# Kernel tuning notes

Measured on AMD Instinct MI355X. Metric: run time of the kernel, lower is better.

## Reference

```python
import jax, jax.numpy as jnp
import numpy as np

B, S, D = 2, 2048, 1024
H, DC = 16, 16          # num_heads, head_coord_dim
CD = 16                 # coord_dim
DH = D // H             # head_dim = 64


def setup_inputs() -> dict:
    key = jax.random.key(0)
    ks = jax.random.split(key, 8)
    s = 0.02
    return {
        "hidden_states": jax.random.normal(ks[0], (B, S, D), jnp.float32),
        "coordinates": jax.random.normal(ks[1], (B, S, CD), jnp.float32),
        "Wv": jax.random.normal(ks[2], (D, D), jnp.float32) * s,
        "bv": jnp.zeros((D,), jnp.float32),
        "Wc": jax.random.normal(ks[3], (H * DC, CD), jnp.float32) * s,
        "bc": jnp.zeros((H * DC,), jnp.float32),
        "Wn": jax.random.normal(ks[4], (CD, D), jnp.float32) * s,
        "bn": jnp.zeros((CD,), jnp.float32),
        "Wo": jax.random.normal(ks[5], (D, D), jnp.float32) * s,
        "bo": jnp.zeros((D,), jnp.float32),
        "gamma": jnp.zeros((1, H, 1, 1), jnp.float32),
    }


def reference(hidden_states, coordinates, Wv, bv, Wc, bc, Wn, bn, Wo, bo, gamma):
    # value: [B,S,D] -> [B,H,S,DH]
    value = (hidden_states @ Wv.T + bv).reshape(B, S, H, DH).transpose(0, 2, 1, 3)
    # coordinate heads: [B,S,CD] -> [B,H,S,DC]
    z = (coordinates @ Wc.T + bc).reshape(B, S, H, DC).transpose(0, 2, 1, 3)
    z_sq = jnp.sum(z * z, axis=-1, keepdims=True)           # [B,H,S,1]
    # pairwise squared distances [B,H,S,S]
    sq_dist = z_sq + jnp.swapaxes(z_sq, -1, -2) - 2.0 * jnp.einsum("bhsc,bhtc->bhst", z, z)
    sq_dist = jnp.maximum(sq_dist, 0.0)
    g = jax.nn.softplus(gamma)                               # [1,H,1,1]
    attn = jax.nn.softmax(-g * sq_dist, axis=-1)             # [B,H,S,S]
    out = jnp.einsum("bhst,bhtd->bhsd", attn, value)         # [B,H,S,DH]
    out = out.transpose(0, 2, 1, 3).reshape(B, S, D)
    updated_hidden = out @ Wo.T + bo
    updated_coords = hidden_states @ Wn.T + bn               # [B,S,CD]
    return updated_hidden, updated_coords
```

## Files before the change

kernel.cpp:

```cpp
#include <hip/hip_runtime.h>
#include <math.h>

typedef short short8 __attribute__((ext_vector_type(8)));
typedef short short4t __attribute__((ext_vector_type(4)));
typedef float f32x4  __attribute__((ext_vector_type(4)));

#define AS1 __attribute__((address_space(1)))
#define AS3 __attribute__((address_space(3)))

__device__ __forceinline__ unsigned cvt_pk_bf16(float lo, float hi) {
    unsigned r;
    asm("v_cvt_pk_bf16_f32 %0, %1, %2" : "=v"(r) : "v"(lo), "v"(hi));
    return r;
}
__device__ __forceinline__ unsigned f2bf_rne(float x) {
    unsigned u = __float_as_uint(x);
    return (u + 0x7fffu + ((u >> 16) & 1u)) >> 16;
}
__device__ __forceinline__ float exp2_fast(float x) {
    float r;
    asm("v_exp_f32 %0, %1" : "=v"(r) : "v"(x));
    return r;
}
__device__ __forceinline__ f32x4 mfma_k16(short4t a, short4t b, f32x4 c) {
#if __has_builtin(__builtin_amdgcn_mfma_f32_16x16x16bf16_1k)
    return __builtin_amdgcn_mfma_f32_16x16x16bf16_1k(a, b, c, 0, 0, 0);
#else
    asm volatile("v_mfma_f32_16x16x16_bf16 %0, %1, %2, %0" : "+v"(c) : "v"(a), "v"(b));
    return c;
#endif
}

__global__ __launch_bounds__(256) void f2bf_kernel(const float* __restrict__ in,
                                                   short* __restrict__ out, int n8) {
    const int i = blockIdx.x * 256 + threadIdx.x;
    if (i >= n8) return;
    const float4 a = ((const float4*)in)[2 * i];
    const float4 b = ((const float4*)in)[2 * i + 1];
    uint4 r;
    r.x = cvt_pk_bf16(a.x, a.y);
    r.y = cvt_pk_bf16(a.z, a.w);
    r.z = cvt_pk_bf16(b.x, b.y);
    r.w = cvt_pk_bf16(b.z, b.w);
    ((uint4*)out)[i] = r;
}

__global__ __launch_bounds__(256) void f2bfW(const float* __restrict__ Wv,
                                             const float* __restrict__ Wo,
                                             const float* __restrict__ Wn,
                                             short* __restrict__ Wvb,
                                             short* __restrict__ Wob,
                                             short* __restrict__ Wnb) {
    const int i = blockIdx.x * 256 + threadIdx.x;
    const float* src;
    short* dst;
    int ii;
    if (i < 131072)      { src = Wv; dst = Wvb; ii = i; }
    else if (i < 262144) { src = Wo; dst = Wob; ii = i - 131072; }
    else                 { src = Wn; dst = Wnb; ii = i - 262144; }
    const float4 a = ((const float4*)src)[2 * ii];
    const float4 b = ((const float4*)src)[2 * ii + 1];
    uint4 r;
    r.x = cvt_pk_bf16(a.x, a.y);
    r.y = cvt_pk_bf16(a.z, a.w);
    r.z = cvt_pk_bf16(b.x, b.y);
    r.w = cvt_pk_bf16(b.z, b.w);
    ((uint4*)dst)[ii] = r;
}

__global__ __launch_bounds__(256) void zker3(const float* __restrict__ coords,
                                             const float* __restrict__ Wc,
                                             const float* __restrict__ bc,
                                             const float* __restrict__ gamma,
                                             short* __restrict__ ZA,
                                             short* __restrict__ ZB) {
    const int bs = blockIdx.x;
    const int b = bs >> 11, s = bs & 2047;
    const int tid = threadIdx.x;
    __shared__ float csh[16];
    if (tid < 16) csh[tid] = coords[(size_t)bs * 16 + tid];
    __syncthreads();
    float z = bc[tid];
#pragma unroll
    for (int k = 0; k < 16; k++) z = fmaf(csh[k], Wc[tid * 16 + k], z);
    const unsigned ub = f2bf_rne(z);
    const float zb = __uint_as_float(ub << 16);
    float sq = zb * zb;
    sq += __shfl_xor(sq, 1, 64);
    sq += __shfl_xor(sq, 2, 64);
    sq += __shfl_xor(sq, 4, 64);
    sq += __shfl_xor(sq, 8, 64);
    const int h = tid >> 4, c = tid & 15;
    const float gm = gamma[h];
    const float sp = fmaxf(gm, 0.f) + log1pf(__expf(-fabsf(gm)));
    const float ch = -sp * 1.4426950408889634f;
    const size_t row = ((size_t)(b * 16 + h) * 2048 + s) * 32;
    ZA[row + c] = (short)ub;
    ZA[row + 16 + c] = (c == 0) ? (short)f2bf_rne(sq)
                                : (c == 1 ? (short)0x3F80 : (short)0);
    ZB[row + c] = (short)f2bf_rne(-2.f * ch * zb);
    ZB[row + 16 + c] = (c == 0) ? (short)f2bf_rne(ch)
                                : (c == 1 ? (short)f2bf_rne(ch * sq) : (short)0);
}

template <int EPI>
__global__ __launch_bounds__(256) void gemm_mfma(const short* __restrict__ A,
                                                 const short* __restrict__ W,
                                                 const float* __restrict__ bias,
                                                 void* __restrict__ Cout) {
    __shared__ short As[2][128][64];
    __shared__ short Bs[2][64][64];
    const int tid = threadIdx.x;
    const int wv = tid >> 6, l = tid & 63, g = l >> 4, qc = l & 15;
    const int wm = wv >> 1, wn = wv & 1;
    const int Mb = blockIdx.y * 128, Nb = blockIdx.x * 64;

    auto stage = [&](int buf, int k0) {
#pragma unroll
        for (int i = 0; i < 4; i++) {
            const int c = i * 256 + tid;
            const int r = c >> 3, jp = c & 7;
            const int js = jp ^ (r & 7);
            const short* gsA = A + (size_t)(Mb + r) * 1024 + k0 + js * 8;
            short* ldsA = &As[buf][0][0] + (size_t)(i * 256 + wv * 64) * 8;
            __builtin_amdgcn_global_load_lds((const AS1 void*)gsA, (AS3 void*)ldsA, 16, 0, 0);
        }
#pragma unroll
        for (int i = 0; i < 2; i++) {
            const int c = i * 256 + tid;
            const int r = c >> 3, jp = c & 7;
            const int js = jp ^ (r & 7);
            const short* gsB = W + (size_t)(Nb + r) * 1024 + k0 + js * 8;
            short* ldsB = &Bs[buf][0][0] + (size_t)(i * 256 + wv * 64) * 8;
            __builtin_amdgcn_global_load_lds((const AS1 void*)gsB, (AS3 void*)ldsB, 16, 0, 0);
        }
    };

    f32x4 acc[4][2] = {};
    stage(0, 0);
    __syncthreads();
    int cur = 0;
#pragma unroll 1
    for (int kb = 0; kb < 16; kb++) {
        if (kb < 15) stage(cur ^ 1, (kb + 1) * 64);
#pragma unroll
        for (int ks = 0; ks < 2; ks++) {
            const int cs = ((ks * 4 + g) ^ (qc & 7)) * 8;
            short8 af[4], bfr[2];
#pragma unroll
            for (int mt = 0; mt < 4; mt++)
                af[mt] = *(const short8*)&As[cur][wm * 64 + mt * 16 + qc][cs];
#pragma unroll
            for (int nt = 0; nt < 2; nt++)
                bfr[nt] = *(const short8*)&Bs[cur][wn * 32 + nt * 16 + qc][cs];
#pragma unroll
            for (int mt = 0; mt < 4; mt++)
#pragma unroll
                for (int nt = 0; nt < 2; nt++)
                    acc[mt][nt] = __builtin_amdgcn_mfma_f32_16x16x32_bf16(af[mt], bfr[nt], acc[mt][nt], 0, 0, 0);
        }
        __syncthreads();
        cur ^= 1;
    }

    float bl[2];
#pragma unroll
    for (int nt = 0; nt < 2; nt++) bl[nt] = bias[Nb + wn * 32 + nt * 16 + qc];
#pragma unroll
    for (int mt = 0; mt < 4; mt++) {
#pragma unroll
        for (int nt = 0; nt < 2; nt++) {
            const int m0 = Mb + wm * 64 + mt * 16 + g * 4;
            const int n  = Nb + wn * 32 + nt * 16 + qc;
            f32x4 v = acc[mt][nt];
            v = v + bl[nt];
            if (EPI == 0) {
                const int bb = m0 >> 11, s0 = m0 & 2047;
                const int hh = n >> 6, dh = n & 63;
                const int s0x = s0 ^ (((n >> 3) & 1) << 2);
                uint2 p2;
                p2.x = cvt_pk_bf16(v[0], v[1]);
                p2.y = cvt_pk_bf16(v[2], v[3]);
                *(uint2*)((short*)Cout + (size_t)((bb * 16 + hh) * 64 + dh) * 2048 + s0x) = p2;
            } else {
                float* C = (float*)Cout;
#pragma unroll
                for (int i = 0; i < 4; i++) C[(size_t)(m0 + i) * 1024 + n] = v[i];
            }
        }
    }
}

__global__ __launch_bounds__(256, 4) void attn_mfma8(const short* __restrict__ ZAg,
                                                     const short* __restrict__ ZBg,
                                                     const short* __restrict__ Vt,
                                                     short* __restrict__ AOb) {
    __shared__ short Vs[2][4096];
    __shared__ short Zs[4][2048];
    const int tid = threadIdx.x;
    const int wv = tid >> 6, l = tid & 63, g = l >> 4, qc = l & 15;
    const int lin = blockIdx.x;
    const int work = (lin & 7) * 128 + (lin >> 3);
    const int qb = work & 31, h = (work >> 5) & 15, b = work >> 9;
    const int bh = b * 16 + h;
    const int q0 = qb * 64 + wv * 16;

    const short* ZAb = ZAg + (size_t)bh * (2048 * 32);
    const short* ZBb = ZBg + (size_t)bh * (2048 * 32);
    const short* Vb  = Vt  + (size_t)bh * (64 * 2048);

    const short8 zq = *(const short8*)(ZBb + (size_t)(q0 + qc) * 32 + g * 8);

    union { unsigned u[2]; short4t s4; } ones4;
    ones4.u[0] = ones4.u[1] = (qc == 0) ? 0x3F803F80u : 0u;

    f32x4 acc[4] = {};
    f32x4 accl = {};

    const short* gvb = Vb + (size_t)l * 2048 + wv * 8;
    short* lvd = &Vs[0][0] + (size_t)tid * 8;
    short* lzd = &Zs[0][0] + (size_t)tid * 8;
    const int z_kt = tid >> 6, z_g = (tid >> 4) & 3, z_r = tid & 15;

    auto stageV = [&](int buf, int kb) {
        const short* gv = gvb + kb;
        short* lvb = lvd + buf * 4096;
        __builtin_amdgcn_global_load_lds((const AS1 void*)gv, (AS3 void*)lvb, 16, 0, 0);
        __builtin_amdgcn_global_load_lds((const AS1 void*)(gv + 32), (AS3 void*)(lvb + 2048), 16, 0, 0);
    };
    auto stageZ = [&](int buf, int kb) {
        const short* gz = ZAb + (size_t)(kb + z_kt * 16 + z_r) * 32 + z_g * 8;
        __builtin_amdgcn_global_load_lds((const AS1 void*)gz, (AS3 void*)(lzd + buf * 2048), 16, 0, 0);
    };

    const int vrd = (((g >> 1) * 64 + qc) * 8) + (((g & 1) ^ ((qc >> 3) & 1)) << 2);
    const int zrd = g * 128 + qc * 8;

    auto computeP = [&](int zbuf, unsigned pko[4][2]) {
        const short* Zc = &Zs[zbuf][0];
        short8 zk[4];
#pragma unroll
        for (int kt = 0; kt < 4; kt++)
            zk[kt] = *(const short8*)(Zc + zrd + kt * 512);
        const f32x4 z4 = {0.f, 0.f, 0.f, 0.f};
#pragma unroll
        for (int kt = 0; kt < 4; kt++) {
            const f32x4 S = __builtin_amdgcn_mfma_f32_16x16x32_bf16(zk[kt], zq, z4, 0, 0, 0);
            pko[kt][0] = cvt_pk_bf16(exp2_fast(fminf(S[0], 0.f)), exp2_fast(fminf(S[1], 0.f)));
            pko[kt][1] = cvt_pk_bf16(exp2_fast(fminf(S[2], 0.f)), exp2_fast(fminf(S[3], 0.f)));
        }
    };

    stageV(0, 0);
    stageZ(0, 0);
    stageZ(1, 64);
    __syncthreads();

    unsigned pk[4][2];
    computeP(0, pk);

    int cur = 0;
#pragma unroll 1
    for (int i = 0; i < 32; i++) {
        const int kb = i * 64;
        if (i < 31) stageV(cur ^ 1, kb + 64);
        if (i < 30) stageZ((i + 2) & 3, kb + 128);

        unsigned pknext[4][2];
        computeP((i + 1) & 3, pknext);

        const short* Vc = &Vs[cur][0];
        __builtin_amdgcn_s_setprio(1);
#pragma unroll
        for (int kt = 0; kt < 4; kt++) {
            union { unsigned u[2]; short4t s4; } pb;
            pb.u[0] = pk[kt][0];
            pb.u[1] = pk[kt][1];
            accl = mfma_k16(ones4.s4, pb.s4, accl);
#pragma unroll
            for (int mt = 0; mt < 4; mt++)
                acc[mt] = mfma_k16(*(const short4t*)(Vc + vrd + kt * 1024 + mt * 128),
                                   pb.s4, acc[mt]);
        }
        __builtin_amdgcn_s_setprio(0);

#pragma unroll
        for (int kt = 0; kt < 4; kt++) {
            pk[kt][0] = pknext[kt][0];
            pk[kt][1] = pknext[kt][1];
        }

        __syncthreads();
        cur ^= 1;
    }

    const float lv2 = __shfl(accl[0], qc, 64);
    const float inv = 1.f / lv2;
    const size_t row = (size_t)(b * 2048 + q0 + qc) * 1024 + h * 64;
#pragma unroll
    for (int mt = 0; mt < 4; mt++) {
        uint2 o;
        o.x = cvt_pk_bf16(acc[mt][0] * inv, acc[mt][1] * inv);
        o.y = cvt_pk_bf16(acc[mt][2] * inv, acc[mt][3] * inv);
        *(uint2*)(AOb + row + mt * 16 + g * 4) = o;
    }
}

__global__ __launch_bounds__(256) void coords_mfma(const short* __restrict__ A,
                                                   const short* __restrict__ Wnb,
                                                   const float* __restrict__ bn,
                                                   float* __restrict__ out1) {
    __shared__ float red[4][16][16];
    const int tid = threadIdx.x;
    const int wv = tid >> 6, l = tid & 63, g = l >> 4, qc = l & 15;
    const int m0 = blockIdx.x * 16;
    const int k0 = wv * 256;
    f32x4 acc = {};
#pragma unroll
    for (int kk = 0; kk < 256; kk += 32) {
        const short8 af = *(const short8*)(A + (size_t)(m0 + qc) * 1024 + k0 + kk + g * 8);
        const short8 bf = *(const short8*)(Wnb + (size_t)qc * 1024 + k0 + kk + g * 8);
        acc = __builtin_amdgcn_mfma_f32_16x16x32_bf16(af, bf, acc, 0, 0, 0);
    }
#pragma unroll
    for (int i2 = 0; i2 < 4; i2++) red[wv][g * 4 + i2][qc] = acc[i2];
    __syncthreads();
    const int r = tid >> 4, c = tid & 15;
    const float s = red[0][r][c] + red[1][r][c] + red[2][r][c] + red[3][r][c] + bn[c];
    out1[(size_t)(m0 + r) * 16 + c] = s;
}

extern "C" void kernel_launch(void* const* d_in, const int* in_sizes, int n_in,
                              void* d_out, int out_size, void* d_ws, size_t ws_size,
                              hipStream_t stream) {
    (void)in_sizes; (void)n_in; (void)out_size; (void)ws_size;
    const float* hidden = (const float*)d_in[0];
    const float* coords = (const float*)d_in[1];
    const float* Wv = (const float*)d_in[2];
    const float* bv = (const float*)d_in[3];
    const float* Wc = (const float*)d_in[4];
    const float* bc = (const float*)d_in[5];
    const float* Wn = (const float*)d_in[6];
    const float* bn = (const float*)d_in[7];
    const float* Wo = (const float*)d_in[8];
    const float* bo = (const float*)d_in[9];
    const float* gamma = (const float*)d_in[10];

    char* wsb = (char*)d_ws;
    short* hsb = (short*)(wsb);
    short* AOb = hsb;
    short* Wvb = (short*)(wsb + (8 << 20));
    short* Wob = (short*)(wsb + (10 << 20));
    short* Vt  = (short*)(wsb + (12 << 20));
    short* ZA  = (short*)(wsb + (20 << 20));
    short* ZB  = (short*)(wsb + (24 << 20));
    short* Wnb = (short*)(wsb + (28 << 20));

    float* out_hidden = (float*)d_out;
    float* out_coords = out_hidden + 4194304;

    f2bf_kernel<<<2048, 256, 0, stream>>>(hidden, hsb, 524288);
    f2bfW<<<1032, 256, 0, stream>>>(Wv, Wo, Wn, Wvb, Wob, Wnb);
    zker3<<<4096, 256, 0, stream>>>(coords, Wc, bc, gamma, ZA, ZB);
    gemm_mfma<0><<<dim3(16, 32), 256, 0, stream>>>(hsb, Wvb, bv, (void*)Vt);
    coords_mfma<<<256, 256, 0, stream>>>(hsb, Wnb, bn, out_coords);
    attn_mfma8<<<1024, 256, 0, stream>>>(ZA, ZB, Vt, AOb);
    gemm_mfma<1><<<dim3(16, 32), 256, 0, stream>>>(AOb, Wob, bo, (void*)out_hidden);
}
```

Before: 107.0 us.

## Split attention over key dimension into two partial blocks plus combine kernel

Splits the attention kernel's key loop into two halves handled by separate blocks, doubling the grid from 1024 to 2048 blocks. Each half writes its unnormalised bf16 partial output and row sum to workspace, and a new combine kernel adds them and normalises. This is meant to fix poor CU occupancy when 1024 blocks fill 256 CUs unevenly; launch bounds also go from 4 to 5 blocks per SM. The cost is extra global traffic for the partials, one more launch, and bf16 rounding of the partial sums. The split path is used only when the workspace is large enough, otherwise it falls back to the unsplit kernel.

Result: slower. 115.0 us (+7.5%).

```diff
diff --git a/kernel.cpp b/kernel.cpp
--- a/kernel.cpp
+++ b/kernel.cpp
@@ -191,19 +191,27 @@
     }
 }
 
-__global__ __launch_bounds__(256, 4) void attn_mfma8(const short* __restrict__ ZAg,
+template <int NSPLIT>
+__global__ __launch_bounds__(256, 5) void attn_mfma9(const short* __restrict__ ZAg,
                                                      const short* __restrict__ ZBg,
                                                      const short* __restrict__ Vt,
-                                                     short* __restrict__ AOb) {
+                                                     short* __restrict__ AOb,
+                                                     short* __restrict__ pacc,
+                                                     float* __restrict__ pl) {
     __shared__ short Vs[2][4096];
     __shared__ short Zs[4][2048];
     const int tid = threadIdx.x;
-    const int wv = tid >> 6, l = tid & 63, g = l >> 4, qc = l & 15;
+    const int wv = tid >> 6, ln = tid & 63, g = ln >> 4, qc = ln & 15;
+    constexpr int NB = 1024 * NSPLIT;
+    constexpr int NIT = 2048 / (64 * NSPLIT);
     const int lin = blockIdx.x;
-    const int work = (lin & 7) * 128 + (lin >> 3);
-    const int qb = work & 31, h = (work >> 5) & 15, b = work >> 9;
+    const int work = (lin & 7) * (NB / 8) + (lin >> 3);
+    const int sp = work >> 10;
+    const int r = work & 1023;
+    const int qb = r & 31, h = (r >> 5) & 15, b = r >> 9;
     const int bh = b * 16 + h;
     const int q0 = qb * 64 + wv * 16;
+    const int kb0 = sp * (2048 / NSPLIT);
 
     const short* ZAb = ZAg + (size_t)bh * (2048 * 32);
     const short* ZBb = ZBg + (size_t)bh * (2048 * 32);
@@ -217,7 +225,7 @@
     f32x4 acc[4] = {};
     f32x4 accl = {};
 
-    const short* gvb = Vb + (size_t)l * 2048 + wv * 8;
+    const short* gvb = Vb + (size_t)ln * 2048 + wv * 8;
     short* lvd = &Vs[0][0] + (size_t)tid * 8;
     short* lzd = &Zs[0][0] + (size_t)tid * 8;
     const int z_kt = tid >> 6, z_g = (tid >> 4) & 3, z_r = tid & 15;
@@ -251,9 +259,9 @@
         }
     };
 
-    stageV(0, 0);
-    stageZ(0, 0);
-    stageZ(1, 64);
+    stageV(0, kb0);
+    stageZ(0, kb0);
+    stageZ(1, kb0 + 64);
     __syncthreads();
 
     unsigned pk[4][2];
@@ -261,10 +269,10 @@
 
     int cur = 0;
 #pragma unroll 1
-    for (int i = 0; i < 32; i++) {
-        const int kb = i * 64;
-        if (i < 31) stageV(cur ^ 1, kb + 64);
-        if (i < 30) stageZ((i + 2) & 3, kb + 128);
+    for (int i = 0; i < NIT; i++) {
+        const int kb = kb0 + i * 64;
+        if (i < NIT - 1) stageV(cur ^ 1, kb + 64);
+        if (i < NIT - 2) stageZ((i + 2) & 3, kb + 128);
 
         unsigned pknext[4][2];
         computeP((i + 1) & 3, pknext);
@@ -294,16 +302,55 @@
         cur ^= 1;
     }
 
-    const float lv2 = __shfl(accl[0], qc, 64);
-    const float inv = 1.f / lv2;
-    const size_t row = (size_t)(b * 2048 + q0 + qc) * 1024 + h * 64;
-#pragma unroll
-    for (int mt = 0; mt < 4; mt++) {
-        uint2 o;
-        o.x = cvt_pk_bf16(acc[mt][0] * inv, acc[mt][1] * inv);
-        o.y = cvt_pk_bf16(acc[mt][2] * inv, acc[mt][3] * inv);
-        *(uint2*)(AOb + row + mt * 16 + g * 4) = o;
-    }
+    if (NSPLIT == 1) {
+        const float lv2 = __shfl(accl[0], qc, 64);
+        const float inv = 1.f / lv2;
+        const size_t row = (size_t)(b * 2048 + q0 + qc) * 1024 + h * 64;
+#pragma unroll
+        for (int mt = 0; mt < 4; mt++) {
+            uint2 o;
+            o.x = cvt_pk_bf16(acc[mt][0] * inv, acc[mt][1] * inv);
+            o.y = cvt_pk_bf16(acc[mt][2] * inv, acc[mt][3] * inv);
+            *(uint2*)(AOb + row + mt * 16 + g * 4) = o;
+        }
+    } else {
+        short* pa = pacc + (size_t)sp * 4194304;
+        const size_t row = (size_t)(b * 2048 + q0 + qc) * 1024 + h * 64;
+#pragma unroll
+        for (int mt = 0; mt < 4; mt++) {
+            uint2 o;
+            o.x = cvt_pk_bf16(acc[mt][0], acc[mt][1]);
+            o.y = cvt_pk_bf16(acc[mt][2], acc[mt][3]);
+            *(uint2*)(pa + row + mt * 16 + g * 4) = o;
+        }
+        if (ln < 16)
+            pl[sp * 65536 + bh * 2048 + q0 + ln] = accl[0];
+    }
+}
+
+__global__ __launch_bounds__(256) void combine2(const short* __restrict__ pacc,
+                                                const float* __restrict__ pl,
+                                                short* __restrict__ AOb) {
+    const int i = blockIdx.x * 256 + threadIdx.x;
+    const int row = i >> 7;
+    const int h = (i >> 3) & 15;
+    const int b = row >> 11, q = row & 2047;
+    const int lidx = (b * 16 + h) * 2048 + q;
+    const float inv = 1.f / (pl[lidx] + pl[65536 + lidx]);
+    const uint4 a0 = ((const uint4*)pacc)[i];
+    const uint4 a1 = ((const uint4*)(pacc + 4194304))[i];
+    uint4 o;
+    const unsigned* u0 = (const unsigned*)&a0;
+    const unsigned* u1 = (const unsigned*)&a1;
+    unsigned* ou = (unsigned*)&o;
+#pragma unroll
+    for (int w = 0; w < 4; w++) {
+        const float lo = (__uint_as_float(u0[w] << 16) + __uint_as_float(u1[w] << 16)) * inv;
+        const float hi = (__uint_as_float(u0[w] & 0xffff0000u) +
+                          __uint_as_float(u1[w] & 0xffff0000u)) * inv;
+        ou[w] = cvt_pk_bf16(lo, hi);
+    }
+    ((uint4*)AOb)[i] = o;
 }
 
 __global__ __launch_bounds__(256) void coords_mfma(const short* __restrict__ A,
@@ -333,7 +380,7 @@
 extern "C" void kernel_launch(void* const* d_in, const int* in_sizes, int n_in,
                               void* d_out, int out_size, void* d_ws, size_t ws_size,
                               hipStream_t stream) {
-    (void)in_sizes; (void)n_in; (void)out_size; (void)ws_size;
+    (void)in_sizes; (void)n_in; (void)out_size;
     const float* hidden = (const float*)d_in[0];
     const float* coords = (const float*)d_in[1];
     const float* Wv = (const float*)d_in[2];
@@ -355,15 +402,24 @@
     short* ZA  = (short*)(wsb + (20 << 20));
     short* ZB  = (short*)(wsb + (24 << 20));
     short* Wnb = (short*)(wsb + (28 << 20));
+    short* pacc = (short*)(wsb + (30 << 20));
+    float* pl   = (float*)(wsb + (46 << 20));
 
     float* out_hidden = (float*)d_out;
     float* out_coords = out_hidden + 4194304;
+
+    const bool split = ws_size >= ((size_t)47 << 20);
 
     f2bf_kernel<<<2048, 256, 0, stream>>>(hidden, hsb, 524288);
     f2bfW<<<1032, 256, 0, stream>>>(Wv, Wo, Wn, Wvb, Wob, Wnb);
     zker3<<<4096, 256, 0, stream>>>(coords, Wc, bc, gamma, ZA, ZB);
     gemm_mfma<0><<<dim3(16, 32), 256, 0, stream>>>(hsb, Wvb, bv, (void*)Vt);
     coords_mfma<<<256, 256, 0, stream>>>(hsb, Wnb, bn, out_coords);
-    attn_mfma8<<<1024, 256, 0, stream>>>(ZA, ZB, Vt, AOb);
+    if (split) {
+        attn_mfma9<2><<<2048, 256, 0, stream>>>(ZA, ZB, Vt, AOb, pacc, pl);
+        combine2<<<2048, 256, 0, stream>>>(pacc, pl, AOb);
+    } else {
+        attn_mfma9<1><<<1024, 256, 0, stream>>>(ZA, ZB, Vt, AOb, pacc, pl);
+    }
     gemm_mfma<1><<<dim3(16, 32), 256, 0, stream>>>(AOb, Wob, bo, (void*)out_hidden);
 }
```
